# Kernel optimization log

Hardware: AMD Instinct MI355X
Metric: run time of the kernel (lower is better)

## Reference

```python
import jax, jax.numpy as jnp
import numpy as np
import math

B, S, D = 2, 2048, 2048
H = 16
HD = D // H          # 128
WINDOW = 256


def setup_inputs() -> dict:
    key = jax.random.key(0)
    ks = jax.random.split(key, 5)
    x = jax.random.normal(ks[0], (B, S, D), dtype=jnp.float32)
    # standard RoPE frequency tables: shape (S, HD//2)
    inv_freq = 1.0 / (10000.0 ** (np.arange(0, HD, 2, dtype=np.float32) / HD))
    t = np.arange(S, dtype=np.float32)
    ang = np.outer(t, inv_freq)  # [S, HD//2]
    freqs_cos = jnp.asarray(np.cos(ang), dtype=jnp.float32)
    freqs_sin = jnp.asarray(np.sin(ang), dtype=jnp.float32)
    scale = 0.02
    wq = jax.random.normal(ks[1], (D, D), dtype=jnp.float32) * scale
    wk = jax.random.normal(ks[2], (D, D), dtype=jnp.float32) * scale
    wv = jax.random.normal(ks[3], (D, D), dtype=jnp.float32) * scale
    wo = jax.random.normal(ks[4], (D, D), dtype=jnp.float32) * scale
    return {"x": x, "freqs_cos": freqs_cos, "freqs_sin": freqs_sin,
            "wq": wq, "wk": wk, "wv": wv, "wo": wo}


def _rope(t, cos, sin):
    # t: [B, S, H, HD]; cos/sin: [S, HD//2]
    tr = t.reshape(t.shape[:-1] + (HD // 2, 2))
    r, i = tr[..., 0], tr[..., 1]
    c = cos[None, :, None, :]
    s = sin[None, :, None, :]
    out_r = r * c - i * s
    out_i = r * s + i * c
    return jnp.stack([out_r, out_i], axis=-1).reshape(t.shape)


def _sliding_window_mask(seqlen, window):
    i = jnp.arange(seqlen)[:, None]
    j = jnp.arange(seqlen)[None, :]
    valid = (j <= i) & (j > i - window)
    return jnp.where(valid, 0.0, -jnp.inf).astype(jnp.float32)  # [S, S]


def reference(x, freqs_cos, freqs_sin, wq, wk, wv, wo):
    bsz, seqlen, _ = x.shape
    # QKV projections (nn.Linear, no bias: y = x @ W^T)
    xq = (x @ wq.T).reshape(bsz, seqlen, H, HD)
    xk = (x @ wk.T).reshape(bsz, seqlen, H, HD)
    xv = (x @ wv.T).reshape(bsz, seqlen, H, HD)
    # RoPE on q and k
    xq = _rope(xq, freqs_cos, freqs_sin)
    xk = _rope(xk, freqs_cos, freqs_sin)
    # [B, H, S, HD]
    q = xq.transpose(0, 2, 1, 3)
    k = xk.transpose(0, 2, 1, 3)
    v = xv.transpose(0, 2, 1, 3)
    mask = _sliding_window_mask(seqlen, WINDOW)  # [S, S]
    scores = jnp.einsum('bhqd,bhkd->bhqk', q, k) / math.sqrt(HD)
    scores = scores + mask[None, None, :, :]
    probs = jax.nn.softmax(scores, axis=-1)
    out = jnp.einsum('bhqk,bhkd->bhqd', probs, v)
    out = out.transpose(0, 2, 1, 3).reshape(bsz, seqlen, H * HD)
    return out @ wo.T
```

## Files before the change

### kernel.cpp

```cpp
#include <hip/hip_runtime.h>

typedef __attribute__((ext_vector_type(8))) short bf16x8;
typedef __attribute__((ext_vector_type(4))) float f32x4;

#define LOG2E 1.4426950408889634f
#define SWZ(L) ((L) ^ ((((L) >> 7) & 7) << 4))

__device__ __forceinline__ unsigned short f2bf(float f) {
  unsigned int x = __builtin_bit_cast(unsigned int, f);
  x += 0x7fffu + ((x >> 16) & 1u);
  return (unsigned short)(x >> 16);
}
__device__ __forceinline__ float bf2f(unsigned short u) {
  unsigned int x = ((unsigned int)u) << 16;
  return __builtin_bit_cast(float, x);
}

__device__ __forceinline__ void gload16(const void* g, void* l) {
  __builtin_amdgcn_global_load_lds((const __attribute__((address_space(1))) void*)g,
                                   (__attribute__((address_space(3))) void*)l, 16, 0, 0);
}

__device__ __forceinline__ bf16x8 ldsf(const char* region, int row, int colbyte) {
  const int L = row * 128 + colbyte;
  return *(const bf16x8*)(region + SWZ(L));
}

__device__ __forceinline__ void stage_half(const unsigned short* __restrict__ G, int rowbase,
                                           int K, int ku, char* region, int w, int l) {
#pragma unroll
  for (int i = 0; i < 2; ++i) {
    const int off = w * 1024 + i * 8192;
    const int P = off + l * 16;
    const int L = SWZ(P);
    const int r = L >> 7, cs = (L & 127) >> 1;
    gload16(G + (long long)(rowbase + r) * K + ku + cs, region + off);
  }
}

__global__ __launch_bounds__(256)
void cast_pack(const float* __restrict__ x, const float* __restrict__ wq,
               const float* __restrict__ wk, const float* __restrict__ wv,
               const float* __restrict__ wo,
               unsigned short* __restrict__ xb, unsigned short* __restrict__ wqkv,
               unsigned short* __restrict__ wob) {
  const int NX = 8388608, DD = 4194304;
  const int i = (blockIdx.x * 256 + threadIdx.x) * 4;
  const float* src; unsigned short* dst; float scale = 1.0f;
  if (i < NX)               { src = x + i;                    dst = xb + i; }
  else if (i < NX + DD)     { int o = i - NX;      src = wq + o; dst = wqkv + o; scale = 0.088388347648318447f; }
  else if (i < NX + 2*DD)   { int o = i - NX - DD;   src = wk + o; dst = wqkv + DD + o; }
  else if (i < NX + 3*DD)   { int o = i - NX - 2*DD; src = wv + o; dst = wqkv + 2*DD + o; }
  else                      { int o = i - NX - 3*DD; src = wo + o; dst = wob + o; }
  const float4 v = *(const float4*)src;
  ushort4 u;
  u.x = f2bf(v.x * scale); u.y = f2bf(v.y * scale);
  u.z = f2bf(v.z * scale); u.w = f2bf(v.w * scale);
  *(ushort4*)dst = u;
}

template<int MODE>
__global__ __launch_bounds__(512, 2)
void gemm256(const unsigned short* __restrict__ A, const unsigned short* __restrict__ Bw,
             float* __restrict__ Of, unsigned short* __restrict__ Qb,
             unsigned short* __restrict__ Kb, unsigned short* __restrict__ Vt,
             const float* __restrict__ fc, const float* __restrict__ fs, int K) {
  __shared__ char lds[98304];
  char* const Abase = lds;
  char* const Bbase = lds + 32768;
  const int tid = threadIdx.x;
  const int l = tid & 63, w = tid >> 6;
  const int wr = w >> 2, wc = w & 3;
  const int lq = l & 15, g = l >> 4;
  const int nwg = gridDim.x;
  const int cpx = nwg >> 3;
  const int orig = blockIdx.x;
  const int wg = (orig & 7) * cpx + (orig >> 3);
  const int bm = wg & 31, bn = wg >> 5;
  const unsigned short* Ab = A + (long long)bm * 128 * K;
  const unsigned short* Bb = Bw + (long long)bn * 256 * K;
  const int NT = K >> 6;

  stage_half(Bb, 0,   K, 0,  Bbase,         w, l);
  stage_half(Bb, 128, K, 0,  Bbase + 16384, w, l);
  stage_half(Ab, 0,   K, 0,  Abase,         w, l);
  stage_half(Bb, 0,   K, 64, Bbase + 32768, w, l);
  stage_half(Bb, 128, K, 64, Bbase + 49152, w, l);
  asm volatile("s_waitcnt vmcnt(4)" ::: "memory");
  __builtin_amdgcn_s_barrier();

  f32x4 acc[4][4] = {};
  const int brow0 = (wc & 1) * 64;
  const int arow0 = wr * 64;
  for (int t = 0; t < NT; ++t) {
    const int d = t & 1;
    const char* Ar = Abase + d * 16384;
    const char* Br = Bbase + d * 32768 + (wc >> 1) * 16384;
    bf16x8 a0, a1, b[2][4];
#pragma unroll
    for (int kk = 0; kk < 2; ++kk)
#pragma unroll
      for (int ni = 0; ni < 4; ++ni)
        b[kk][ni] = ldsf(Br, brow0 + ni * 16 + lq, kk * 64 + g * 16);
    a0 = ldsf(Ar, arow0 + 0 * 16 + lq, g * 16);
    a1 = ldsf(Ar, arow0 + 1 * 16 + lq, g * 16);
    { const int u = t + 1; const int ku = (u < NT) ? u * 64 : 0;
      stage_half(Ab, 0, K, ku, Abase + (u & 1) * 16384, w, l); }
    asm volatile("s_waitcnt lgkmcnt(0)" ::: "memory");
    __builtin_amdgcn_sched_barrier(0);
    __builtin_amdgcn_s_setprio(1);
#pragma unroll
    for (int ni = 0; ni < 4; ++ni) {
      acc[0][ni] = __builtin_amdgcn_mfma_f32_16x16x32_bf16(a0, b[0][ni], acc[0][ni], 0, 0, 0);
      acc[1][ni] = __builtin_amdgcn_mfma_f32_16x16x32_bf16(a1, b[0][ni], acc[1][ni], 0, 0, 0);
    }
    __builtin_amdgcn_s_setprio(0);
    __builtin_amdgcn_s_barrier();
    a0 = ldsf(Ar, arow0 + 2 * 16 + lq, g * 16);
    a1 = ldsf(Ar, arow0 + 3 * 16 + lq, g * 16);
    { const int u = t + 2; const int ku = (u < NT) ? u * 64 : 0;
      stage_half(Bb, 0, K, ku, Bbase + d * 32768, w, l); }
    asm volatile("s_waitcnt lgkmcnt(0)" ::: "memory");
    __builtin_amdgcn_sched_barrier(0);
    __builtin_amdgcn_s_setprio(1);
#pragma unroll
    for (int ni = 0; ni < 4; ++ni) {
      acc[2][ni] = __builtin_amdgcn_mfma_f32_16x16x32_bf16(a0, b[0][ni], acc[2][ni], 0, 0, 0);
      acc[3][ni] = __builtin_amdgcn_mfma_f32_16x16x32_bf16(a1, b[0][ni], acc[3][ni], 0, 0, 0);
    }
    __builtin_amdgcn_s_setprio(0);
    __builtin_amdgcn_s_barrier();
    a0 = ldsf(Ar, arow0 + 0 * 16 + lq, 64 + g * 16);
    a1 = ldsf(Ar, arow0 + 1 * 16 + lq, 64 + g * 16);
    { const int u = t + 2; const int ku = (u < NT) ? u * 64 : 0;
      stage_half(Bb, 128, K, ku, Bbase + d * 32768 + 16384, w, l); }
    asm volatile("s_waitcnt lgkmcnt(0)" ::: "memory");
    __builtin_amdgcn_sched_barrier(0);
    __builtin_amdgcn_s_setprio(1);
#pragma unroll
    for (int ni = 0; ni < 4; ++ni) {
      acc[0][ni] = __builtin_amdgcn_mfma_f32_16x16x32_bf16(a0, b[1][ni], acc[0][ni], 0, 0, 0);
      acc[1][ni] = __builtin_amdgcn_mfma_f32_16x16x32_bf16(a1, b[1][ni], acc[1][ni], 0, 0, 0);
    }
    __builtin_amdgcn_s_setprio(0);
    __builtin_amdgcn_s_barrier();
    a0 = ldsf(Ar, arow0 + 2 * 16 + lq, 64 + g * 16);
    a1 = ldsf(Ar, arow0 + 3 * 16 + lq, 64 + g * 16);
    asm volatile("s_waitcnt lgkmcnt(0)" ::: "memory");
    __builtin_amdgcn_sched_barrier(0);
    __builtin_amdgcn_s_setprio(1);
#pragma unroll
    for (int ni = 0; ni < 4; ++ni) {
      acc[2][ni] = __builtin_amdgcn_mfma_f32_16x16x32_bf16(a0, b[1][ni], acc[2][ni], 0, 0, 0);
      acc[3][ni] = __builtin_amdgcn_mfma_f32_16x16x32_bf16(a1, b[1][ni], acc[3][ni], 0, 0, 0);
    }
    __builtin_amdgcn_s_setprio(0);
    asm volatile("s_waitcnt vmcnt(4)" ::: "memory");
    __builtin_amdgcn_s_barrier();
  }
  asm volatile("s_waitcnt vmcnt(0)" ::: "memory");

  if (MODE == 0) {
    const int colb = bn * 256;
    if (colb < 4096) {
      unsigned short* dst = (colb < 2048) ? Qb : Kb;
      const int cb = colb & 2047;
#pragma unroll
      for (int mi = 0; mi < 4; ++mi) {
        const int row = bm * 128 + wr * 64 + mi * 16 + g * 4;
        const int s0 = row & 2047;
#pragma unroll
        for (int ni = 0; ni < 4; ++ni) {
          const int col = cb + wc * 64 + ni * 16 + lq;
          const int hd = col & 127;
          const int j = hd >> 1;
          const bool odd = hd & 1;
#pragma unroll
          for (int r = 0; r < 4; ++r) {
            const int s = s0 + r;
            const float c  = fc[s * 64 + j];
            const float sn = fs[s * 64 + j];
            const float own = acc[mi][ni][r];
            const float oth = __shfl_xor(own, 1);
            const float val = odd ? (oth * sn + own * c) : (own * c - oth * sn);
            dst[(long long)(row + r) * 2048 + col] = f2bf(val);
          }
        }
      }
    } else {
#pragma unroll
      for (int mi = 0; mi < 4; ++mi) {
        const int row = bm * 128 + wr * 64 + mi * 16 + g * 4;
        const int b = row >> 11, s = row & 2047;
#pragma unroll
        for (int ni = 0; ni < 4; ++ni) {
          const int c = colb - 4096 + wc * 64 + ni * 16 + lq;
          const int h = c >> 7, dd = c & 127;
          ushort4 o4;
          o4.x = f2bf(acc[mi][ni][0]); o4.y = f2bf(acc[mi][ni][1]);
          o4.z = f2bf(acc[mi][ni][2]); o4.w = f2bf(acc[mi][ni][3]);
          *(ushort4*)&Vt[((long long)((b * 16 + h) * 128 + dd)) * 2048 + s] = o4;
        }
      }
    }
  } else {
#pragma unroll
    for (int mi = 0; mi < 4; ++mi) {
      const int row = bm * 128 + wr * 64 + mi * 16 + g * 4;
#pragma unroll
      for (int ni = 0; ni < 4; ++ni) {
        const int col = bn * 256 + wc * 64 + ni * 16 + lq;
#pragma unroll
        for (int r = 0; r < 4; ++r)
          Of[(long long)(row + r) * 2048 + col] = acc[mi][ni][r];
      }
    }
  }
}

__global__ __launch_bounds__(256)
void attn_k(const unsigned short* __restrict__ Qb, const unsigned short* __restrict__ Kb,
            const unsigned short* __restrict__ Vt, unsigned short* __restrict__ Ob) {
  __shared__ unsigned short plds[8192];
  const int tid = threadIdx.x;
  const int l = tid & 63, w = tid >> 6;
  const int lq = l & 15, g = l >> 4;
  const int qb = blockIdx.x, bh = blockIdx.y;
  const int b = bh >> 4, h = bh & 15;
  const int q_abs = qb * 64 + w * 16 + lq;
  const unsigned short* Qrow = Qb + ((long long)(b * 2048 + q_abs)) * 2048 + h * 128;
  bf16x8 qf[4];
#pragma unroll
  for (int ks = 0; ks < 4; ++ks)
    qf[ks] = *(const bf16x8*)&Qrow[ks * 32 + g * 8];
  f32x4 o[8] = {};
  float m = -1e30f, lsum = 0.0f;
  char* pb = (char*)(plds + w * 2048);
  const unsigned short* Kbase = Kb + ((long long)(b * 2048)) * 2048 + h * 128;
  const unsigned short* Vbase = Vt + ((long long)bh) * 128 * 2048;
  const int kb_lo = (qb >= 4) ? qb - 4 : 0;
  for (int kb = kb_lo; kb <= qb; kb += 2) {
    const bool hb = (kb + 1 <= qb);
    const int key0 = kb * 64;
    float sva[16], svb[16];
    {
      f32x4 sc[4] = {};
      __builtin_amdgcn_s_setprio(1);
#pragma unroll
      for (int mt = 0; mt < 4; ++mt) {
        const unsigned short* Krow = Kbase + (long long)(key0 + mt * 16 + lq) * 2048;
#pragma unroll
        for (int ks = 0; ks < 4; ++ks) {
          const bf16x8 kf = *(const bf16x8*)&Krow[ks * 32 + g * 8];
          sc[mt] = __builtin_amdgcn_mfma_f32_16x16x32_bf16(kf, qf[ks], sc[mt], 0, 0, 0);
        }
      }
      __builtin_amdgcn_s_setprio(0);
#pragma unroll
      for (int mt = 0; mt < 4; ++mt)
#pragma unroll
        for (int r = 0; r < 4; ++r) {
          const int key = key0 + mt * 16 + g * 4 + r;
          const bool valid = (key <= q_abs) && (key + 256 > q_abs);
          sva[mt * 4 + r] = valid ? sc[mt][r] : -1e30f;
        }
    }
    if (hb) {
      f32x4 sc[4] = {};
      __builtin_amdgcn_s_setprio(1);
#pragma unroll
      for (int mt = 0; mt < 4; ++mt) {
        const unsigned short* Krow = Kbase + (long long)(key0 + 64 + mt * 16 + lq) * 2048;
#pragma unroll
        for (int ks = 0; ks < 4; ++ks) {
          const bf16x8 kf = *(const bf16x8*)&Krow[ks * 32 + g * 8];
          sc[mt] = __builtin_amdgcn_mfma_f32_16x16x32_bf16(kf, qf[ks], sc[mt], 0, 0, 0);
        }
      }
      __builtin_amdgcn_s_setprio(0);
#pragma unroll
      for (int mt = 0; mt < 4; ++mt)
#pragma unroll
        for (int r = 0; r < 4; ++r) {
          const int key = key0 + 64 + mt * 16 + g * 4 + r;
          const bool valid = (key <= q_abs) && (key + 256 > q_abs);
          svb[mt * 4 + r] = valid ? sc[mt][r] : -1e30f;
        }
    } else {
#pragma unroll
      for (int i = 0; i < 16; ++i) svb[i] = -1e30f;
    }
    float bmax = -1e30f;
#pragma unroll
    for (int i = 0; i < 16; ++i) bmax = fmaxf(bmax, fmaxf(sva[i], svb[i]));
    bmax = fmaxf(bmax, __shfl_xor(bmax, 16));
    bmax = fmaxf(bmax, __shfl_xor(bmax, 32));
    const float mnew = fmaxf(m, bmax);
    float psum = 0.0f;
#pragma unroll
    for (int i = 0; i < 16; ++i) {
      const float p = __builtin_exp2f((sva[i] - mnew) * LOG2E);
      sva[i] = p; psum += p;
    }
#pragma unroll
    for (int i = 0; i < 16; ++i) {
      const float p = __builtin_exp2f((svb[i] - mnew) * LOG2E);
      svb[i] = p; psum += p;
    }
    psum += __shfl_xor(psum, 16);
    psum += __shfl_xor(psum, 32);
    if (mnew > m) {
      const float rf = __builtin_exp2f((m - mnew) * LOG2E);
      lsum = lsum * rf + psum;
      m = mnew;
#pragma unroll
      for (int dt = 0; dt < 8; ++dt) o[dt] *= rf;
    } else {
      lsum += psum;
    }
#pragma unroll
    for (int mt = 0; mt < 4; ++mt) {
      const unsigned int lo = (unsigned int)f2bf(sva[mt * 4 + 0]) | ((unsigned int)f2bf(sva[mt * 4 + 1]) << 16);
      const unsigned int hi = (unsigned int)f2bf(sva[mt * 4 + 2]) | ((unsigned int)f2bf(sva[mt * 4 + 3]) << 16);
      int byte = lq * 128 + (mt * 16 + g * 4) * 2;
      byte ^= (lq & 7) << 4;
      *(uint2*)(pb + byte) = make_uint2(lo, hi);
    }
    if (hb) {
#pragma unroll
      for (int mt = 0; mt < 4; ++mt) {
        const unsigned int lo = (unsigned int)f2bf(svb[mt * 4 + 0]) | ((unsigned int)f2bf(svb[mt * 4 + 1]) << 16);
        const unsigned int hi = (unsigned int)f2bf(svb[mt * 4 + 2]) | ((unsigned int)f2bf(svb[mt * 4 + 3]) << 16);
        int byte = lq * 128 + (mt * 16 + g * 4) * 2;
        byte ^= (lq & 7) << 4;
        *(uint2*)(pb + 2048 + byte) = make_uint2(lo, hi);
      }
    }
    asm volatile("s_waitcnt lgkmcnt(0)" ::: "memory");
    __builtin_amdgcn_sched_barrier(0);
    bf16x8 pfa[2], pfb[2];
#pragma unroll
    for (int k2 = 0; k2 < 2; ++k2) {
      int byte = lq * 128 + k2 * 64 + g * 16;
      byte ^= (lq & 7) << 4;
      pfa[k2] = *(const bf16x8*)(pb + byte);
      if (hb) pfb[k2] = *(const bf16x8*)(pb + 2048 + byte);
    }
    asm volatile("s_waitcnt lgkmcnt(0)" ::: "memory");
    __builtin_amdgcn_sched_barrier(0);
    __builtin_amdgcn_s_setprio(1);
#pragma unroll
    for (int dt = 0; dt < 8; ++dt) {
      const unsigned short* Vrow = Vbase + (long long)(dt * 16 + lq) * 2048 + key0;
#pragma unroll
      for (int k2 = 0; k2 < 2; ++k2) {
        const bf16x8 vf = *(const bf16x8*)&Vrow[k2 * 32 + g * 8];
        o[dt] = __builtin_amdgcn_mfma_f32_16x16x32_bf16(vf, pfa[k2], o[dt], 0, 0, 0);
      }
      if (hb) {
#pragma unroll
        for (int k2 = 0; k2 < 2; ++k2) {
          const bf16x8 vf = *(const bf16x8*)&Vrow[64 + k2 * 32 + g * 8];
          o[dt] = __builtin_amdgcn_mfma_f32_16x16x32_bf16(vf, pfb[k2], o[dt], 0, 0, 0);
        }
      }
    }
    __builtin_amdgcn_s_setprio(0);
  }
  const float inv = 1.0f / lsum;
  unsigned short* Or = Ob + ((long long)(b * 2048 + q_abs)) * 2048 + h * 128;
#pragma unroll
  for (int dt = 0; dt < 8; ++dt) {
    ushort4 o4;
    o4.x = f2bf(o[dt][0] * inv);
    o4.y = f2bf(o[dt][1] * inv);
    o4.z = f2bf(o[dt][2] * inv);
    o4.w = f2bf(o[dt][3] * inv);
    *(ushort4*)&Or[dt * 16 + g * 4] = o4;
  }
}

extern "C" void kernel_launch(void* const* d_in, const int* in_sizes, int n_in,
                              void* d_out, int out_size, void* d_ws, size_t ws_size,
                              hipStream_t stream) {
  const float* x  = (const float*)d_in[0];
  const float* fc = (const float*)d_in[1];
  const float* fs = (const float*)d_in[2];
  const float* wq = (const float*)d_in[3];
  const float* wk = (const float*)d_in[4];
  const float* wv = (const float*)d_in[5];
  const float* wo = (const float*)d_in[6];

  unsigned short* ws   = (unsigned short*)d_ws;
  unsigned short* xb   = ws;
  unsigned short* wqkv = xb + 8388608;
  unsigned short* wob  = wqkv + 12582912;
  unsigned short* Qb   = wob + 4194304;
  unsigned short* Kb   = Qb + 8388608;
  unsigned short* Vt   = Kb + 8388608;
  unsigned short* Ob   = Vt + 8388608;

  cast_pack<<<24576, 256, 0, stream>>>(x, wq, wk, wv, wo, xb, wqkv, wob);
  gemm256<0><<<768, 512, 0, stream>>>(xb, wqkv, nullptr, Qb, Kb, Vt, fc, fs, 2048);
  attn_k<<<dim3(32, 32), 256, 0, stream>>>(Qb, Kb, Vt, Ob);
  gemm256<1><<<256, 512, 0, stream>>>(Ob, wob, (float*)d_out, nullptr, nullptr, nullptr, fc, fs, 2048);
}
```

Measured before the change: 257.8 us.

## Load GEMM A operand straight into double-buffered registers, bypassing LDS

Each wave now loads its A-operand fragments directly from global memory into two register buffers that alternate, prefetching the next K-tile. Before, A was staged through LDS. LDS use drops from 96KB to 64KB, and each tile needs fewer barriers because only B is still staged through shared memory. In exchange, A rows are fetched redundantly by the waves that share them, and the extra 64 registers per lane raise register pressure under the 512x2 launch bound, which may cause spills.

```diff
diff --git a/kernel.cpp b/kernel.cpp
--- a/kernel.cpp
+++ b/kernel.cpp
@@ -65,9 +65,8 @@
              float* __restrict__ Of, unsigned short* __restrict__ Qb,
              unsigned short* __restrict__ Kb, unsigned short* __restrict__ Vt,
              const float* __restrict__ fc, const float* __restrict__ fs, int K) {
-  __shared__ char lds[98304];
-  char* const Abase = lds;
-  char* const Bbase = lds + 32768;
+  __shared__ char lds[65536];
+  char* const Bbase = lds;
   const int tid = threadIdx.x;
   const int l = tid & 63, w = tid >> 6;
   const int wr = w >> 2, wc = w & 3;
@@ -80,84 +79,70 @@
   const unsigned short* Ab = A + (long long)bm * 128 * K;
   const unsigned short* Bb = Bw + (long long)bn * 256 * K;
   const int NT = K >> 6;
-
+  const int brow0 = (wc & 1) * 64;
+  const int arow0 = wr * 64;
+  const unsigned short* Alane = Ab + (long long)(arow0 + lq) * K + g * 8;
+
+  bf16x8 aA[4][2], aB[4][2];
+#pragma unroll
+  for (int mi = 0; mi < 4; ++mi)
+#pragma unroll
+    for (int kk = 0; kk < 2; ++kk)
+      aA[mi][kk] = *(const bf16x8*)(Alane + (long long)mi * 16 * K + kk * 32);
   stage_half(Bb, 0,   K, 0,  Bbase,         w, l);
   stage_half(Bb, 128, K, 0,  Bbase + 16384, w, l);
-  stage_half(Ab, 0,   K, 0,  Abase,         w, l);
   stage_half(Bb, 0,   K, 64, Bbase + 32768, w, l);
   stage_half(Bb, 128, K, 64, Bbase + 49152, w, l);
   asm volatile("s_waitcnt vmcnt(4)" ::: "memory");
   __builtin_amdgcn_s_barrier();
 
   f32x4 acc[4][4] = {};
-  const int brow0 = (wc & 1) * 64;
-  const int arow0 = wr * 64;
-  for (int t = 0; t < NT; ++t) {
-    const int d = t & 1;
-    const char* Ar = Abase + d * 16384;
-    const char* Br = Bbase + d * 32768 + (wc >> 1) * 16384;
-    bf16x8 a0, a1, b[2][4];
-#pragma unroll
-    for (int kk = 0; kk < 2; ++kk)
-#pragma unroll
-      for (int ni = 0; ni < 4; ++ni)
-        b[kk][ni] = ldsf(Br, brow0 + ni * 16 + lq, kk * 64 + g * 16);
-    a0 = ldsf(Ar, arow0 + 0 * 16 + lq, g * 16);
-    a1 = ldsf(Ar, arow0 + 1 * 16 + lq, g * 16);
-    { const int u = t + 1; const int ku = (u < NT) ? u * 64 : 0;
-      stage_half(Ab, 0, K, ku, Abase + (u & 1) * 16384, w, l); }
-    asm volatile("s_waitcnt lgkmcnt(0)" ::: "memory");
-    __builtin_amdgcn_sched_barrier(0);
-    __builtin_amdgcn_s_setprio(1);
-#pragma unroll
-    for (int ni = 0; ni < 4; ++ni) {
-      acc[0][ni] = __builtin_amdgcn_mfma_f32_16x16x32_bf16(a0, b[0][ni], acc[0][ni], 0, 0, 0);
-      acc[1][ni] = __builtin_amdgcn_mfma_f32_16x16x32_bf16(a1, b[0][ni], acc[1][ni], 0, 0, 0);
-    }
-    __builtin_amdgcn_s_setprio(0);
-    __builtin_amdgcn_s_barrier();
-    a0 = ldsf(Ar, arow0 + 2 * 16 + lq, g * 16);
-    a1 = ldsf(Ar, arow0 + 3 * 16 + lq, g * 16);
-    { const int u = t + 2; const int ku = (u < NT) ? u * 64 : 0;
-      stage_half(Bb, 0, K, ku, Bbase + d * 32768, w, l); }
-    asm volatile("s_waitcnt lgkmcnt(0)" ::: "memory");
-    __builtin_amdgcn_sched_barrier(0);
-    __builtin_amdgcn_s_setprio(1);
-#pragma unroll
-    for (int ni = 0; ni < 4; ++ni) {
-      acc[2][ni] = __builtin_amdgcn_mfma_f32_16x16x32_bf16(a0, b[0][ni], acc[2][ni], 0, 0, 0);
-      acc[3][ni] = __builtin_amdgcn_mfma_f32_16x16x32_bf16(a1, b[0][ni], acc[3][ni], 0, 0, 0);
-    }
-    __builtin_amdgcn_s_setprio(0);
-    __builtin_amdgcn_s_barrier();
-    a0 = ldsf(Ar, arow0 + 0 * 16 + lq, 64 + g * 16);
-    a1 = ldsf(Ar, arow0 + 1 * 16 + lq, 64 + g * 16);
-    { const int u = t + 2; const int ku = (u < NT) ? u * 64 : 0;
-      stage_half(Bb, 128, K, ku, Bbase + d * 32768 + 16384, w, l); }
-    asm volatile("s_waitcnt lgkmcnt(0)" ::: "memory");
-    __builtin_amdgcn_sched_barrier(0);
-    __builtin_amdgcn_s_setprio(1);
-#pragma unroll
-    for (int ni = 0; ni < 4; ++ni) {
-      acc[0][ni] = __builtin_amdgcn_mfma_f32_16x16x32_bf16(a0, b[1][ni], acc[0][ni], 0, 0, 0);
-      acc[1][ni] = __builtin_amdgcn_mfma_f32_16x16x32_bf16(a1, b[1][ni], acc[1][ni], 0, 0, 0);
-    }
-    __builtin_amdgcn_s_setprio(0);
-    __builtin_amdgcn_s_barrier();
-    a0 = ldsf(Ar, arow0 + 2 * 16 + lq, 64 + g * 16);
-    a1 = ldsf(Ar, arow0 + 3 * 16 + lq, 64 + g * 16);
-    asm volatile("s_waitcnt lgkmcnt(0)" ::: "memory");
-    __builtin_amdgcn_sched_barrier(0);
-    __builtin_amdgcn_s_setprio(1);
-#pragma unroll
-    for (int ni = 0; ni < 4; ++ni) {
-      acc[2][ni] = __builtin_amdgcn_mfma_f32_16x16x32_bf16(a0, b[1][ni], acc[2][ni], 0, 0, 0);
-      acc[3][ni] = __builtin_amdgcn_mfma_f32_16x16x32_bf16(a1, b[1][ni], acc[3][ni], 0, 0, 0);
-    }
-    __builtin_amdgcn_s_setprio(0);
-    asm volatile("s_waitcnt vmcnt(4)" ::: "memory");
-    __builtin_amdgcn_s_barrier();
-  }
+
+#define GEMM_TILE(T, ACUR, ANXT)                                                                       \
+  {                                                                                                    \
+    const int d_ = (T) & 1;                                                                            \
+    const char* Br = Bbase + d_ * 32768 + (wc >> 1) * 16384;                                           \
+    bf16x8 b[2][4];                                                                                    \
+    _Pragma("unroll") for (int kk = 0; kk < 2; ++kk)                                                   \
+      _Pragma("unroll") for (int ni = 0; ni < 4; ++ni)                                                 \
+        b[kk][ni] = ldsf(Br, brow0 + ni * 16 + lq, kk * 64 + g * 16);                                  \
+    { const int u_ = (T) + 1; const long long ku_ = (u_ < NT) ? (long long)u_ * 64 : 0;                \
+      _Pragma("unroll") for (int mi = 0; mi < 4; ++mi)                                                 \
+        _Pragma("unroll") for (int kk = 0; kk < 2; ++kk)                                               \
+          ANXT[mi][kk] = *(const bf16x8*)(Alane + (long long)mi * 16 * K + ku_ + kk * 32); }           \
+    asm volatile("s_waitcnt lgkmcnt(0)" ::: "memory");                                                 \
+    __builtin_amdgcn_sched_barrier(0);                                                                 \
+    __builtin_amdgcn_s_setprio(1);                                                                     \
+    _Pragma("unroll") for (int ni = 0; ni < 4; ++ni) {                                                 \
+      acc[0][ni] = __builtin_amdgcn_mfma_f32_16x16x32_bf16(ACUR[0][0], b[0][ni], acc[0][ni], 0, 0, 0); \
+      acc[1][ni] = __builtin_amdgcn_mfma_f32_16x16x32_bf16(ACUR[1][0], b[0][ni], acc[1][ni], 0, 0, 0); \
+    }                                                                                                  \
+    __builtin_amdgcn_s_setprio(0);                                                                     \
+    __builtin_amdgcn_s_barrier();                                                                      \
+    { const int u_ = (T) + 2; const int ku_ = (u_ < NT) ? u_ * 64 : 0;                                 \
+      stage_half(Bb, 0,   K, ku_, Bbase + d_ * 32768, w, l);                                           \
+      stage_half(Bb, 128, K, ku_, Bbase + d_ * 32768 + 16384, w, l); }                                 \
+    __builtin_amdgcn_s_setprio(1);                                                                     \
+    _Pragma("unroll") for (int ni = 0; ni < 4; ++ni) {                                                 \
+      acc[2][ni] = __builtin_amdgcn_mfma_f32_16x16x32_bf16(ACUR[2][0], b[0][ni], acc[2][ni], 0, 0, 0); \
+      acc[3][ni] = __builtin_amdgcn_mfma_f32_16x16x32_bf16(ACUR[3][0], b[0][ni], acc[3][ni], 0, 0, 0); \
+    }                                                                                                  \
+    _Pragma("unroll") for (int ni = 0; ni < 4; ++ni) {                                                 \
+      acc[0][ni] = __builtin_amdgcn_mfma_f32_16x16x32_bf16(ACUR[0][1], b[1][ni], acc[0][ni], 0, 0, 0); \
+      acc[1][ni] = __builtin_amdgcn_mfma_f32_16x16x32_bf16(ACUR[1][1], b[1][ni], acc[1][ni], 0, 0, 0); \
+      acc[2][ni] = __builtin_amdgcn_mfma_f32_16x16x32_bf16(ACUR[2][1], b[1][ni], acc[2][ni], 0, 0, 0); \
+      acc[3][ni] = __builtin_amdgcn_mfma_f32_16x16x32_bf16(ACUR[3][1], b[1][ni], acc[3][ni], 0, 0, 0); \
+    }                                                                                                  \
+    __builtin_amdgcn_s_setprio(0);                                                                     \
+    asm volatile("s_waitcnt vmcnt(4)" ::: "memory");                                                   \
+    __builtin_amdgcn_s_barrier();                                                                      \
+  }
+
+  for (int t = 0; t < NT; t += 2) {
+    GEMM_TILE(t, aA, aB);
+    GEMM_TILE(t + 1, aB, aA);
+  }
+#undef GEMM_TILE
   asm volatile("s_waitcnt vmcnt(0)" ::: "memory");
 
   if (MODE == 0) {
```

After: 444.9 us. +72.6%, slower.

## Stage K and V tiles through shared LDS in attention kernel

Applied to the files above, without the earlier changes.

The attention kernel now loads each 64-key K and V tile cooperatively into swizzled LDS with global_load_lds, then reads MFMA operands from LDS, instead of having each wave fetch K and V rows directly from global memory. The four waves share the same key tiles, so this cuts redundant global and L2 traffic. In exchange it adds 64KB of shared memory per block, which lowers occupancy, plus two barriers per iteration and a full vmcnt wait with no double buffering, so load latency is no longer overlapped with compute.

```diff
diff --git a/kernel.cpp b/kernel.cpp
--- a/kernel.cpp
+++ b/kernel.cpp
@@ -5,6 +5,7 @@
 
 #define LOG2E 1.4426950408889634f
 #define SWZ(L) ((L) ^ ((((L) >> 7) & 7) << 4))
+#define SWZK(L) ((L) ^ ((((L) >> 8) & 7) << 4))
 
 __device__ __forceinline__ unsigned short f2bf(float f) {
   unsigned int x = __builtin_bit_cast(unsigned int, f);
@@ -24,6 +25,10 @@
 __device__ __forceinline__ bf16x8 ldsf(const char* region, int row, int colbyte) {
   const int L = row * 128 + colbyte;
   return *(const bf16x8*)(region + SWZ(L));
+}
+__device__ __forceinline__ bf16x8 ldsfK(const char* region, int row, int colbyte) {
+  const int L = row * 256 + colbyte;
+  return *(const bf16x8*)(region + SWZK(L));
 }
 
 __device__ __forceinline__ void stage_half(const unsigned short* __restrict__ G, int rowbase,
@@ -221,6 +226,8 @@
 __global__ __launch_bounds__(256)
 void attn_k(const unsigned short* __restrict__ Qb, const unsigned short* __restrict__ Kb,
             const unsigned short* __restrict__ Vt, unsigned short* __restrict__ Ob) {
+  __shared__ char kl[32768];
+  __shared__ char vl[32768];
   __shared__ unsigned short plds[8192];
   const int tid = threadIdx.x;
   const int l = tid & 63, w = tid >> 6;
@@ -236,25 +243,56 @@
   f32x4 o[8] = {};
   float m = -1e30f, lsum = 0.0f;
   char* pb = (char*)(plds + w * 2048);
-  const unsigned short* Kbase = Kb + ((long long)(b * 2048)) * 2048 + h * 128;
+  const unsigned short* Kpanel = Kb + ((long long)(b * 2048)) * 2048 + h * 128;
   const unsigned short* Vbase = Vt + ((long long)bh) * 128 * 2048;
   const int kb_lo = (qb >= 4) ? qb - 4 : 0;
   for (int kb = kb_lo; kb <= qb; kb += 2) {
     const bool hb = (kb + 1 <= qb);
     const int key0 = kb * 64;
+    __builtin_amdgcn_s_barrier();
+#pragma unroll
+    for (int i = 0; i < 4; ++i) {
+      const int off = i * 4096 + w * 1024;
+      const int P = off + l * 16;
+      const int L = SWZK(P);
+      gload16(Kpanel + (long long)(key0 + (L >> 8)) * 2048 + ((L & 255) >> 1), kl + off);
+    }
+#pragma unroll
+    for (int i = 0; i < 4; ++i) {
+      const int off = i * 4096 + w * 1024;
+      const int P = off + l * 16;
+      const int L = SWZ(P);
+      gload16(Vbase + (long long)(L >> 7) * 2048 + key0 + ((L & 127) >> 1), vl + off);
+    }
+    if (hb) {
+#pragma unroll
+      for (int i = 0; i < 4; ++i) {
+        const int off = i * 4096 + w * 1024;
+        const int P = off + l * 16;
+        const int L = SWZK(P);
+        gload16(Kpanel + (long long)(key0 + 64 + (L >> 8)) * 2048 + ((L & 255) >> 1), kl + 16384 + off);
+      }
+#pragma unroll
+      for (int i = 0; i < 4; ++i) {
+        const int off = i * 4096 + w * 1024;
+        const int P = off + l * 16;
+        const int L = SWZ(P);
+        gload16(Vbase + (long long)(L >> 7) * 2048 + key0 + 64 + ((L & 127) >> 1), vl + 16384 + off);
+      }
+    }
+    asm volatile("s_waitcnt vmcnt(0)" ::: "memory");
+    __builtin_amdgcn_s_barrier();
     float sva[16], svb[16];
     {
       f32x4 sc[4] = {};
       __builtin_amdgcn_s_setprio(1);
 #pragma unroll
-      for (int mt = 0; mt < 4; ++mt) {
-        const unsigned short* Krow = Kbase + (long long)(key0 + mt * 16 + lq) * 2048;
+      for (int mt = 0; mt < 4; ++mt)
 #pragma unroll
         for (int ks = 0; ks < 4; ++ks) {
-          const bf16x8 kf = *(const bf16x8*)&Krow[ks * 32 + g * 8];
+          const bf16x8 kf = ldsfK(kl, mt * 16 + lq, ks * 64 + g * 16);
           sc[mt] = __builtin_amdgcn_mfma_f32_16x16x32_bf16(kf, qf[ks], sc[mt], 0, 0, 0);
         }
-      }
       __builtin_amdgcn_s_setprio(0);
 #pragma unroll
       for (int mt = 0; mt < 4; ++mt)
@@ -269,14 +307,12 @@
       f32x4 sc[4] = {};
       __builtin_amdgcn_s_setprio(1);
 #pragma unroll
-      for (int mt = 0; mt < 4; ++mt) {
-        const unsigned short* Krow = Kbase + (long long)(key0 + 64 + mt * 16 + lq) * 2048;
+      for (int mt = 0; mt < 4; ++mt)
 #pragma unroll
         for (int ks = 0; ks < 4; ++ks) {
-          const bf16x8 kf = *(const bf16x8*)&Krow[ks * 32 + g * 8];
+          const bf16x8 kf = ldsfK(kl + 16384, mt * 16 + lq, ks * 64 + g * 16);
           sc[mt] = __builtin_amdgcn_mfma_f32_16x16x32_bf16(kf, qf[ks], sc[mt], 0, 0, 0);
         }
-      }
       __builtin_amdgcn_s_setprio(0);
 #pragma unroll
       for (int mt = 0; mt < 4; ++mt)
@@ -351,16 +387,15 @@
     __builtin_amdgcn_s_setprio(1);
 #pragma unroll
     for (int dt = 0; dt < 8; ++dt) {
-      const unsigned short* Vrow = Vbase + (long long)(dt * 16 + lq) * 2048 + key0;
 #pragma unroll
       for (int k2 = 0; k2 < 2; ++k2) {
-        const bf16x8 vf = *(const bf16x8*)&Vrow[k2 * 32 + g * 8];
+        const bf16x8 vf = ldsf(vl, dt * 16 + lq, k2 * 64 + g * 16);
         o[dt] = __builtin_amdgcn_mfma_f32_16x16x32_bf16(vf, pfa[k2], o[dt], 0, 0, 0);
       }
       if (hb) {
 #pragma unroll
         for (int k2 = 0; k2 < 2; ++k2) {
-          const bf16x8 vf = *(const bf16x8*)&Vrow[64 + k2 * 32 + g * 8];
+          const bf16x8 vf = ldsf(vl + 16384, dt * 16 + lq, k2 * 64 + g * 16);
           o[dt] = __builtin_amdgcn_mfma_f32_16x16x32_bf16(vf, pfb[k2], o[dt], 0, 0, 0);
         }
       }
```

Result: faster. 211.9 us, median of 2 (-17.8%).
